# Kernel tuning notes

Hardware: AMD Instinct MI355X
Metric: run time of the kernel (lower is better)

## Reference

```python
import jax, jax.numpy as jnp
import numpy as np

STRIDE = 1
PAD = 3
DIL = 1


def setup_inputs() -> dict:
    key = jax.random.key(0)
    k1, k2, k3 = jax.random.split(key, 3)
    B, C, H, W = 8, 256, 64, 64
    G, K = 4, 7
    Ho, Wo = 64, 64  # same-padding, stride 1
    return {
        "input": jax.random.normal(k1, (B, C, H, W), dtype=jnp.float32),
        "weight": jax.random.normal(k2, (B, G, K, K, Ho, Wo), dtype=jnp.float32),
        "bias": jax.random.normal(k3, (C,), dtype=jnp.float32),
    }


def reference(input, weight, bias):
    # input: [B,C,H,W], weight: [B,G,Kh,Kw,Ho,Wo], bias: [C]
    B, C, H, W = input.shape
    G, Kh, Kw, Ho, Wo = weight.shape[1:]
    Cpg = C // G
    xp = jnp.pad(input, ((0, 0), (0, 0), (PAD, PAD), (PAD, PAD)))
    # group view: [B, G, C/G, H+2p, W+2p]
    xg = xp.reshape(B, G, Cpg, H + 2 * PAD, W + 2 * PAD)
    out = jnp.zeros((B, G, Cpg, Ho, Wo), dtype=input.dtype)
    # fused accumulation over the K*K kernel taps; no im2col blowup
    for kh in range(Kh):
        for kw in range(Kw):
            h0 = kh * DIL
            w0 = kw * DIL
            patch = xg[:, :, :, h0:h0 + Ho * STRIDE:STRIDE, w0:w0 + Wo * STRIDE:STRIDE]
            out = out + patch * weight[:, :, kh, kw][:, :, None, :, :]
    out = out.reshape(B, C, Ho, Wo) + bias[None, :, None, None]
    return out
```

## Files before the change

kernel.cpp:

```cpp
#include <hip/hip_runtime.h>


#define BLK_X 16
#define BLK_Y 8
#define NTHR (BLK_X * BLK_Y)
#define STG_ROWS 14
#define STG_COLS 70
#define STG_N (STG_ROWS * STG_COLS)
#define LDS_STRIDE 71
#define NSTG 8
#define CH_PER_BLK 16

__global__ __launch_bounds__(NTHR, 2)
void involution_kernel(const float* __restrict__ in,
                       const float* __restrict__ w,
                       const float* __restrict__ bias,
                       float* __restrict__ out) {
    __shared__ float lds[STG_ROWS * LDS_STRIDE];

    const int tx = threadIdx.x;
    const int ty = threadIdx.y;
    const int tid = ty * BLK_X + tx;
    const int x0 = tx * 4;
    const int Y0 = blockIdx.x * BLK_Y;
    const int y  = Y0 + ty;
    const int c0 = blockIdx.y * CH_PER_BLK;
    const int bz = blockIdx.z;
    const int g  = bz & 3;

    float4 w4[49];
    const float* wb = w + (size_t)bz * 49 * 4096 + y * 64 + x0;
    #pragma unroll
    for (int k = 0; k < 49; ++k) {
        w4[k] = *(const float4*)(wb + (size_t)k * 4096);
    }

    const float* inb  = in  + (size_t)bz * 64 * 4096;
    float*       outb = out + (size_t)bz * 64 * 4096;

    float stg[NSTG];

    auto load_c = [&](int c, float* r) {
        const float* p = inb + (size_t)c * 4096;
        #pragma unroll
        for (int j = 0; j < NSTG; ++j) {
            int i = tid + j * NTHR;
            float v = 0.f;
            if (i < STG_N) {
                int rr = i / STG_COLS;
                int cc = i - rr * STG_COLS;
                int gy = Y0 + rr - 3;
                int gx = cc - 3;
                if (gy >= 0 && gy < 64 && gx >= 0 && gx < 64)
                    v = p[gy * 64 + gx];
            }
            r[j] = v;
        }
    };
    auto write_stage = [&](const float* r) {
        #pragma unroll
        for (int j = 0; j < NSTG; ++j) {
            int i = tid + j * NTHR;
            if (i < STG_N) {
                int rr = i / STG_COLS;
                int cc = i - rr * STG_COLS;
                lds[rr * LDS_STRIDE + cc] = r[j];
            }
        }
    };

    load_c(c0, stg);
    write_stage(stg);
    __syncthreads();

    for (int cc = 0; cc < CH_PER_BLK; ++cc) {
        const int c = c0 + cc;

        float nstg[NSTG];
        if (cc + 1 < CH_PER_BLK) load_c(c + 1, nstg);

        float acc0 = 0.f, acc1 = 0.f, acc2 = 0.f, acc3 = 0.f;
        #pragma unroll
        for (int kh = 0; kh < 7; ++kh) {
            const float* lrow = &lds[(ty + kh) * LDS_STRIDE + x0];
            float vals[10];
            #pragma unroll
            for (int j = 0; j < 10; ++j) vals[j] = lrow[j];
            #pragma unroll
            for (int kw = 0; kw < 7; ++kw) {
                const float4 wv = w4[kh * 7 + kw];
                acc0 += vals[kw + 0] * wv.x;
                acc1 += vals[kw + 1] * wv.y;
                acc2 += vals[kw + 2] * wv.z;
                acc3 += vals[kw + 3] * wv.w;
            }
        }

        const float bv = bias[g * 64 + c];
        float4 o;
        o.x = acc0 + bv; o.y = acc1 + bv; o.z = acc2 + bv; o.w = acc3 + bv;
        *(float4*)(outb + (size_t)c * 4096 + y * 64 + x0) = o;

        if (cc + 1 < CH_PER_BLK) {
            __syncthreads();
            write_stage(nstg);
            __syncthreads();
        }
    }
}

extern "C" void kernel_launch(void* const* d_in, const int* in_sizes, int n_in,
                              void* d_out, int out_size, void* d_ws, size_t ws_size,
                              hipStream_t stream) {
    const float* in   = (const float*)d_in[0];
    const float* wgt  = (const float*)d_in[1];
    const float* bias = (const float*)d_in[2];
    float* out = (float*)d_out;

    dim3 block(BLK_X, BLK_Y, 1);
    dim3 grid(64 / BLK_Y, 64 / CH_PER_BLK, 32);
    involution_kernel<<<grid, block, 0, stream>>>(in, wgt, bias, out);
}
```

Before: 126.8 us.

## Stage eight channels in LDS at once and stream weights per tap

The kernel no longer keeps all 49 weight float4s in registers and walking 16 channels through a double-buffered LDS tile with per-channel barriers. Each block now loads eight channels' halo tiles (16 rows tall) into LDS in one pass with a single barrier. Each weight float4 is then loaded once per tap from global memory and reused across the eight channel accumulators. This removes the repeated syncs and the register pressure of the weight array, and the LDS reads become vectorised. In exchange, each block reads the weights once per eight channels instead of once per sixteen, which doubles total weight traffic, and the staging load no longer overlaps with compute.

```diff
diff --git a/kernel.cpp b/kernel.cpp
--- a/kernel.cpp
+++ b/kernel.cpp
@@ -2,110 +2,94 @@
 
 
 #define BLK_X 16
-#define BLK_Y 8
+#define BLK_Y 16
 #define NTHR (BLK_X * BLK_Y)
-#define STG_ROWS 14
+#define NC 8
+#define TILE_Y 16
+#define STG_ROWS (TILE_Y + 6)
 #define STG_COLS 70
-#define STG_N (STG_ROWS * STG_COLS)
-#define LDS_STRIDE 71
-#define NSTG 8
-#define CH_PER_BLK 16
+#define LDS_STRIDE 72
+#define STG_N (NC * STG_ROWS * STG_COLS)
 
-__global__ __launch_bounds__(NTHR, 2)
+__global__ __launch_bounds__(NTHR, 3)
 void involution_kernel(const float* __restrict__ in,
                        const float* __restrict__ w,
                        const float* __restrict__ bias,
                        float* __restrict__ out) {
-    __shared__ float lds[STG_ROWS * LDS_STRIDE];
+    __shared__ float lds[NC * STG_ROWS * LDS_STRIDE];
 
     const int tx = threadIdx.x;
     const int ty = threadIdx.y;
     const int tid = ty * BLK_X + tx;
     const int x0 = tx * 4;
-    const int Y0 = blockIdx.x * BLK_Y;
+    const int Y0 = blockIdx.x * TILE_Y;
     const int y  = Y0 + ty;
-    const int c0 = blockIdx.y * CH_PER_BLK;
+    const int c0 = blockIdx.y * NC;
     const int bz = blockIdx.z;
     const int g  = bz & 3;
 
-    float4 w4[49];
-    const float* wb = w + (size_t)bz * 49 * 4096 + y * 64 + x0;
+    const float* inb = in + (size_t)bz * 64 * 4096 + (size_t)c0 * 4096;
+
     #pragma unroll
-    for (int k = 0; k < 49; ++k) {
-        w4[k] = *(const float4*)(wb + (size_t)k * 4096);
+    for (int j = 0; j < (STG_N + NTHR - 1) / NTHR; ++j) {
+        int i = tid + j * NTHR;
+        if (i < STG_N) {
+            int ci  = i / (STG_ROWS * STG_COLS);
+            int rem = i - ci * (STG_ROWS * STG_COLS);
+            int rr  = rem / STG_COLS;
+            int cc  = rem - rr * STG_COLS;
+            int gy  = Y0 + rr - 3;
+            int gx  = cc - 3;
+            float v = 0.f;
+            if (gy >= 0 && gy < 64 && gx >= 0 && gx < 64)
+                v = inb[ci * 4096 + gy * 64 + gx];
+            lds[(ci * STG_ROWS + rr) * LDS_STRIDE + cc] = v;
+        }
+    }
+    __syncthreads();
+
+    float acc[NC][4];
+    #pragma unroll
+    for (int ci = 0; ci < NC; ++ci) {
+        acc[ci][0] = 0.f; acc[ci][1] = 0.f; acc[ci][2] = 0.f; acc[ci][3] = 0.f;
     }
 
-    const float* inb  = in  + (size_t)bz * 64 * 4096;
-    float*       outb = out + (size_t)bz * 64 * 4096;
+    const float* wb = w + (size_t)bz * 49 * 4096 + y * 64 + x0;
 
-    float stg[NSTG];
-
-    auto load_c = [&](int c, float* r) {
-        const float* p = inb + (size_t)c * 4096;
+    #pragma unroll
+    for (int kh = 0; kh < 7; ++kh) {
+        float vals[NC][10];
         #pragma unroll
-        for (int j = 0; j < NSTG; ++j) {
-            int i = tid + j * NTHR;
-            float v = 0.f;
-            if (i < STG_N) {
-                int rr = i / STG_COLS;
-                int cc = i - rr * STG_COLS;
-                int gy = Y0 + rr - 3;
-                int gx = cc - 3;
-                if (gy >= 0 && gy < 64 && gx >= 0 && gx < 64)
-                    v = p[gy * 64 + gx];
-            }
-            r[j] = v;
+        for (int ci = 0; ci < NC; ++ci) {
+            const float* lr = &lds[(ci * STG_ROWS + ty + kh) * LDS_STRIDE + x0];
+            float4 a = *(const float4*)lr;
+            float4 b = *(const float4*)(lr + 4);
+            float2 c = *(const float2*)(lr + 8);
+            vals[ci][0] = a.x; vals[ci][1] = a.y; vals[ci][2] = a.z; vals[ci][3] = a.w;
+            vals[ci][4] = b.x; vals[ci][5] = b.y; vals[ci][6] = b.z; vals[ci][7] = b.w;
+            vals[ci][8] = c.x; vals[ci][9] = c.y;
         }
-    };
-    auto write_stage = [&](const float* r) {
         #pragma unroll
-        for (int j = 0; j < NSTG; ++j) {
-            int i = tid + j * NTHR;
-            if (i < STG_N) {
-                int rr = i / STG_COLS;
-                int cc = i - rr * STG_COLS;
-                lds[rr * LDS_STRIDE + cc] = r[j];
+        for (int kw = 0; kw < 7; ++kw) {
+            const float4 wv = *(const float4*)(wb + (size_t)(kh * 7 + kw) * 4096);
+            #pragma unroll
+            for (int ci = 0; ci < NC; ++ci) {
+                acc[ci][0] += vals[ci][kw + 0] * wv.x;
+                acc[ci][1] += vals[ci][kw + 1] * wv.y;
+                acc[ci][2] += vals[ci][kw + 2] * wv.z;
+                acc[ci][3] += vals[ci][kw + 3] * wv.w;
             }
         }
-    };
+    }
 
-    load_c(c0, stg);
-    write_stage(stg);
-    __syncthreads();
-
-    for (int cc = 0; cc < CH_PER_BLK; ++cc) {
-        const int c = c0 + cc;
-
-        float nstg[NSTG];
-        if (cc + 1 < CH_PER_BLK) load_c(c + 1, nstg);
-
-        float acc0 = 0.f, acc1 = 0.f, acc2 = 0.f, acc3 = 0.f;
-        #pragma unroll
-        for (int kh = 0; kh < 7; ++kh) {
-            const float* lrow = &lds[(ty + kh) * LDS_STRIDE + x0];
-            float vals[10];
-            #pragma unroll
-            for (int j = 0; j < 10; ++j) vals[j] = lrow[j];
-            #pragma unroll
-            for (int kw = 0; kw < 7; ++kw) {
-                const float4 wv = w4[kh * 7 + kw];
-                acc0 += vals[kw + 0] * wv.x;
-                acc1 += vals[kw + 1] * wv.y;
-                acc2 += vals[kw + 2] * wv.z;
-                acc3 += vals[kw + 3] * wv.w;
-            }
-        }
-
-        const float bv = bias[g * 64 + c];
+    float* outb = out + (size_t)bz * 64 * 4096 + (size_t)c0 * 4096 + y * 64 + x0;
+    #pragma unroll
+    for (int ci = 0; ci < NC; ++ci) {
+        const float bv = bias[g * 64 + c0 + ci];
         float4 o;
-        o.x = acc0 + bv; o.y = acc1 + bv; o.z = acc2 + bv; o.w = acc3 + bv;
-        *(float4*)(outb + (size_t)c * 4096 + y * 64 + x0) = o;
-
-        if (cc + 1 < CH_PER_BLK) {
-            __syncthreads();
-            write_stage(nstg);
-            __syncthreads();
-        }
+        o.x = acc[ci][0] + bv; o.y = acc[ci][1] + bv;
+        o.z = acc[ci][2] + bv; o.w = acc[ci][3] + bv;
+        *(float4*)(outb + (size_t)ci * 4096) = o;
     }
 }
 
@@ -118,6 +102,6 @@
     float* out = (float*)d_out;
 
     dim3 block(BLK_X, BLK_Y, 1);
-    dim3 grid(64 / BLK_Y, 64 / CH_PER_BLK, 32);
+    dim3 grid(64 / TILE_Y, 64 / NC, 32);
     involution_kernel<<<grid, block, 0, stream>>>(in, wgt, bias, out);
 }
```

New measurement: 155.8 us. 1.23x slower.
